# Kernel tuning notes

Hardware: AMD Instinct MI355X
Metric: run time of the kernel (lower is better)

## Reference

```python
import jax, jax.numpy as jnp
import numpy as np

T, B, I, H = 2048, 4096, 3, 5  # seq_len, batch, input_size, hidden_size (from module)


def setup_inputs() -> dict:
    key = jax.random.key(0)
    ks = jax.random.split(key, 10)
    k = 1.0 / np.sqrt(H)  # torch nn.RNN default init bound
    u = lambda kk, shape: jax.random.uniform(kk, shape, jnp.float32, -k, k)
    return {
        "x": jax.random.normal(ks[0], (T, B, I), jnp.float32),
        "hx": jax.random.normal(ks[1], (2, B, H), jnp.float32),
        "w_ih0": u(ks[2], (H, I)),
        "w_hh0": u(ks[3], (H, H)),
        "b_ih0": u(ks[4], (H,)),
        "b_hh0": u(ks[5], (H,)),
        "w_ih1": u(ks[6], (H, H)),
        "w_hh1": u(ks[7], (H, H)),
        "b_ih1": u(ks[8], (H,)),
        "b_hh1": u(ks[9], (H,)),
    }


def reference(x, hx, w_ih0, w_hh0, b_ih0, b_hh0, w_ih1, w_hh1, b_ih1, b_hh1):
    # Precompute layer-0 input projections for all timesteps in one big GEMM.
    pre0 = jnp.einsum("tbi,hi->tbh", x, w_ih0) + b_ih0  # [T, B, H]

    def step(carry, p0_t):
        h0, h1 = carry
        h0 = jnp.tanh(p0_t + h0 @ w_hh0.T + b_hh0)
        h1 = jnp.tanh(h0 @ w_ih1.T + b_ih1 + h1 @ w_hh1.T + b_hh1)
        return (h0, h1), h1

    (h0_f, h1_f), out = jax.lax.scan(step, (hx[0], hx[1]), pre0)
    h_n = jnp.stack([h0_f, h1_f])  # [2, B, H]
    return out, h_n
```

## Files before the change

### kernel.cpp

```cpp
#include <hip/hip_runtime.h>


typedef float v2f  __attribute__((ext_vector_type(2)));
typedef float v2fu __attribute__((ext_vector_type(2), aligned(4)));
typedef float v3fu __attribute__((ext_vector_type(3), aligned(4)));

#define SEQ_T 2048
#define BATCH 4096
#define ISZ 3
#define HSZ 5
#define TBLK 8
#define NSUP (SEQ_T / TBLK)
#define XSTRIDE (BATCH * ISZ)
#define OSTRIDE (BATCH * HSZ)

template<int K>
__device__ __forceinline__ float qbcast(float v) {
    return __int_as_float(__builtin_amdgcn_mov_dpp(
        __float_as_int(v), K * 0x55, 0xF, 0xF, false));
}
__device__ __forceinline__ v2f vsplat(float s) { return (v2f){s, s}; }
__device__ __forceinline__ v2f vfma(float s, v2f w, v2f a) {
    return __builtin_elementwise_fma(vsplat(s), w, a);
}

__global__ __launch_bounds__(128, 1)
void rnn2_pc(const float* __restrict__ x, const float* __restrict__ hx,
             const float* __restrict__ w_ih0, const float* __restrict__ w_hh0,
             const float* __restrict__ b_ih0, const float* __restrict__ b_hh0,
             const float* __restrict__ w_ih1, const float* __restrict__ w_hh1,
             const float* __restrict__ b_ih1, const float* __restrict__ b_hh1,
             float* __restrict__ out)
{
    __shared__ float ring[2][TBLK][16][12];

    const int tid  = threadIdx.x;
    const int wid  = tid >> 6;
    const int lane = tid & 63;
    const int cl   = lane >> 2;
    const int ja   = lane & 3;
    const int jb   = ja + 1;
    const int c    = blockIdx.x * 16 + cl;
    const float S  = 2.8853900817779268f;

    const v2f bias0p = (v2f){ S * (b_ih0[ja] + b_hh0[ja]), S * (b_ih0[jb] + b_hh0[jb]) };
    const v2f bias1p = (v2f){ S * (b_ih1[ja] + b_hh1[ja]), S * (b_ih1[jb] + b_hh1[jb]) };
#define LW(W, k, n)  (v2f){ S * W[ja * (n) + (k)], S * W[jb * (n) + (k)] }
    const v2f wi0p0 = LW(w_ih0, 0, ISZ), wi0p1 = LW(w_ih0, 1, ISZ), wi0p2 = LW(w_ih0, 2, ISZ);
    const v2f wh0p0 = LW(w_hh0, 0, HSZ), wh0p1 = LW(w_hh0, 1, HSZ), wh0p2 = LW(w_hh0, 2, HSZ),
              wh0p3 = LW(w_hh0, 3, HSZ), wh0p4 = LW(w_hh0, 4, HSZ);
    const v2f wi1p0 = LW(w_ih1, 0, HSZ), wi1p1 = LW(w_ih1, 1, HSZ), wi1p2 = LW(w_ih1, 2, HSZ),
              wi1p3 = LW(w_ih1, 3, HSZ), wi1p4 = LW(w_ih1, 4, HSZ);
    const v2f wh1p0 = LW(w_hh1, 0, HSZ), wh1p1 = LW(w_hh1, 1, HSZ), wh1p2 = LW(w_hh1, 2, HSZ),
              wh1p3 = LW(w_hh1, 3, HSZ), wh1p4 = LW(w_hh1, 4, HSZ);
#undef LW

    float h0b0 = hx[(size_t)c * HSZ + 0], h0b1 = hx[(size_t)c * HSZ + 1],
          h0b2 = hx[(size_t)c * HSZ + 2], h0b3 = hx[(size_t)c * HSZ + 3],
          h0b4 = hx[(size_t)c * HSZ + 4];
    const size_t hb1 = (size_t)BATCH * HSZ + (size_t)c * HSZ;
    float h1b0 = hx[hb1 + 0], h1b1 = hx[hb1 + 1], h1b2 = hx[hb1 + 2],
          h1b3 = hx[hb1 + 3], h1b4 = hx[hb1 + 4];

    unsigned xoff = (unsigned)c * ISZ;
    v3fu xA0, xA1, xA2, xA3, xA4, xA5, xA6, xA7;
    v3fu xB0, xB1, xB2, xB3, xB4, xB5, xB6, xB7;
#define LOADX(P)                                                           \
    {                                                                      \
        P##0 = *(const v3fu*)(x + xoff + 0*XSTRIDE);                       \
        P##1 = *(const v3fu*)(x + xoff + 1*XSTRIDE);                       \
        P##2 = *(const v3fu*)(x + xoff + 2*XSTRIDE);                       \
        P##3 = *(const v3fu*)(x + xoff + 3*XSTRIDE);                       \
        P##4 = *(const v3fu*)(x + xoff + 4*XSTRIDE);                       \
        P##5 = *(const v3fu*)(x + xoff + 5*XSTRIDE);                       \
        P##6 = *(const v3fu*)(x + xoff + 6*XSTRIDE);                       \
        P##7 = *(const v3fu*)(x + xoff + 7*XSTRIDE);                       \
        xoff += 8u * XSTRIDE;                                              \
    }

    unsigned ooff = (unsigned)c * HSZ + (unsigned)ja;
    float g0, g1, g2, g3, g4;

#define STEP0(XV, WR, TT)                                                  \
    {                                                                      \
        v2f a = bias0p, cc = (v2f){0.0f, 0.0f};                            \
        a  = vfma(XV.x,  wi0p0, a);                                        \
        cc = vfma(XV.y,  wi0p1, cc);                                       \
        a  = vfma(XV.z,  wi0p2, a);                                        \
        cc = vfma(h0b0, wh0p0, cc);                                        \
        a  = vfma(h0b1, wh0p1, a);                                         \
        cc = vfma(h0b2, wh0p2, cc);                                        \
        a  = vfma(h0b3, wh0p3, a);                                         \
        cc = vfma(h0b4, wh0p4, cc);                                        \
        a = a + cc;                                                        \
        v2f e0;                                                            \
        e0.x = __builtin_amdgcn_exp2f(a.x);                                \
        e0.y = __builtin_amdgcn_exp2f(a.y);                                \
        const v2f p0 = e0 + vsplat(1.0f);                                  \
        v2f r0;                                                            \
        r0.x = __builtin_amdgcn_rcpf(p0.x);                                \
        r0.y = __builtin_amdgcn_rcpf(p0.y);                                \
        const v2f n0 = __builtin_elementwise_fma(vsplat(-2.0f), r0, vsplat(1.0f)); \
        h0b0 = qbcast<0>(n0.x);                                            \
        h0b1 = qbcast<1>(n0.x);                                            \
        h0b2 = qbcast<2>(n0.x);                                            \
        h0b3 = qbcast<3>(n0.x);                                            \
        h0b4 = qbcast<3>(n0.y);                                            \
        *(v2f*)&WR[TT][cl][ja * 2] = n0;                                   \
    }

#define PBLOCK(P, RB)                                                      \
    {                                                                      \
        float (*wr)[16][12] = ring[RB];                                    \
        STEP0(P##0, wr, 0)                                                 \
        STEP0(P##1, wr, 1)                                                 \
        STEP0(P##2, wr, 2)                                                 \
        STEP0(P##3, wr, 3)                                                 \
        STEP0(P##4, wr, 4)                                                 \
        STEP0(P##5, wr, 5)                                                 \
        STEP0(P##6, wr, 6)                                                 \
        STEP0(P##7, wr, 7)                                                 \
    }

#define STEP1(RD, TT, DOPRE)                                               \
    {                                                                      \
        const float u0 = g0, u1 = g1, u2 = g2, u3 = g3, u4 = g4;           \
        if (DOPRE) {                                                       \
            g0 = RD[(TT) + 1][cl][0];                                      \
            g1 = RD[(TT) + 1][cl][2];                                      \
            g2 = RD[(TT) + 1][cl][4];                                      \
            g3 = RD[(TT) + 1][cl][6];                                      \
            g4 = RD[(TT) + 1][cl][7];                                      \
        }                                                                  \
        v2f d = bias1p, ee = (v2f){0.0f, 0.0f};                            \
        d  = vfma(u0,   wi1p0, d);                                         \
        ee = vfma(u1,   wi1p1, ee);                                        \
        d  = vfma(u2,   wi1p2, d);                                         \
        ee = vfma(u3,   wi1p3, ee);                                        \
        d  = vfma(u4,   wi1p4, d);                                         \
        ee = vfma(h1b0, wh1p0, ee);                                        \
        d  = vfma(h1b1, wh1p1, d);                                         \
        ee = vfma(h1b2, wh1p2, ee);                                        \
        d  = vfma(h1b3, wh1p3, d);                                         \
        ee = vfma(h1b4, wh1p4, ee);                                        \
        d = d + ee;                                                        \
        v2f e1;                                                            \
        e1.x = __builtin_amdgcn_exp2f(d.x);                                \
        e1.y = __builtin_amdgcn_exp2f(d.y);                                \
        const v2f p1 = e1 + vsplat(1.0f);                                  \
        v2f r1;                                                            \
        r1.x = __builtin_amdgcn_rcpf(p1.x);                                \
        r1.y = __builtin_amdgcn_rcpf(p1.y);                                \
        const v2f n1 = __builtin_elementwise_fma(vsplat(-2.0f), r1, vsplat(1.0f)); \
        *(v2fu*)(out + ooff) = n1;                                         \
        ooff += OSTRIDE;                                                   \
        h1b0 = qbcast<0>(n1.x);                                            \
        h1b1 = qbcast<1>(n1.x);                                            \
        h1b2 = qbcast<2>(n1.x);                                            \
        h1b3 = qbcast<3>(n1.x);                                            \
        h1b4 = qbcast<3>(n1.y);                                            \
    }

#define CBLOCK(RB)                                                         \
    {                                                                      \
        const float (*rd)[16][12] = ring[RB];                              \
        g0 = rd[0][cl][0];                                                 \
        g1 = rd[0][cl][2];                                                 \
        g2 = rd[0][cl][4];                                                 \
        g3 = rd[0][cl][6];                                                 \
        g4 = rd[0][cl][7];                                                 \
        STEP1(rd, 0, 1)                                                    \
        STEP1(rd, 1, 1)                                                    \
        STEP1(rd, 2, 1)                                                    \
        STEP1(rd, 3, 1)                                                    \
        STEP1(rd, 4, 1)                                                    \
        STEP1(rd, 5, 1)                                                    \
        STEP1(rd, 6, 1)                                                    \
        STEP1(rd, 7, 0)                                                    \
    }

    LOADX(xA)

    __syncthreads();
    if (wid == 0) { LOADX(xB) PBLOCK(xA, 0) }

    for (int sp = 0; sp < 127; ++sp) {
        __syncthreads();
        if (wid == 0) { LOADX(xA) PBLOCK(xB, 1) } else { CBLOCK(0) }
        __syncthreads();
        if (wid == 0) { LOADX(xB) PBLOCK(xA, 0) } else { CBLOCK(1) }
    }

    __syncthreads();
    if (wid == 0) { PBLOCK(xB, 1) } else { CBLOCK(0) }

    __syncthreads();
    if (wid != 0) { CBLOCK(1) }

#undef STEP0
#undef STEP1
#undef PBLOCK
#undef CBLOCK
#undef LOADX

    float* hn = out + (size_t)SEQ_T * BATCH * HSZ;
    if (wid == 0) {
        hn[(size_t)c * HSZ + 0] = h0b0;
        hn[(size_t)c * HSZ + 1] = h0b1;
        hn[(size_t)c * HSZ + 2] = h0b2;
        hn[(size_t)c * HSZ + 3] = h0b3;
        hn[(size_t)c * HSZ + 4] = h0b4;
    } else {
        hn[hb1 + 0] = h1b0;
        hn[hb1 + 1] = h1b1;
        hn[hb1 + 2] = h1b2;
        hn[hb1 + 3] = h1b3;
        hn[hb1 + 4] = h1b4;
    }
}

extern "C" void kernel_launch(void* const* d_in, const int* in_sizes, int n_in,
                              void* d_out, int out_size, void* d_ws, size_t ws_size,
                              hipStream_t stream) {
    rnn2_pc<<<BATCH / 16, 128, 0, stream>>>(
        (const float*)d_in[0], (const float*)d_in[1],
        (const float*)d_in[2], (const float*)d_in[3],
        (const float*)d_in[4], (const float*)d_in[5],
        (const float*)d_in[6], (const float*)d_in[7],
        (const float*)d_in[8], (const float*)d_in[9],
        (float*)d_out);
}
```

Before: 403.7 us.

## Defer layer-1 output stores and double-buffer vectorized LDS prefetch

The layer-1 consumer wave now keeps each block's eight output vectors in registers and writes them to global memory at the start of the next block, so the stores no longer sit inside the serial recurrence chain. The LDS reads of layer-0 hidden states are also reorganized: three 2-wide loads replace five scalar loads, and two register sets alternate so the prefetch runs two steps ahead. This shortens the critical path per timestep at the cost of extra registers and a bunched burst of stores per block.

```diff
diff --git a/kernel.cpp b/kernel.cpp
--- a/kernel.cpp
+++ b/kernel.cpp
@@ -10,7 +10,6 @@
 #define ISZ 3
 #define HSZ 5
 #define TBLK 8
-#define NSUP (SEQ_T / TBLK)
 #define XSTRIDE (BATCH * ISZ)
 #define OSTRIDE (BATCH * HSZ)
 
@@ -25,12 +24,12 @@
 }
 
 __global__ __launch_bounds__(128, 1)
-void rnn2_pc(const float* __restrict__ x, const float* __restrict__ hx,
-             const float* __restrict__ w_ih0, const float* __restrict__ w_hh0,
-             const float* __restrict__ b_ih0, const float* __restrict__ b_hh0,
-             const float* __restrict__ w_ih1, const float* __restrict__ w_hh1,
-             const float* __restrict__ b_ih1, const float* __restrict__ b_hh1,
-             float* __restrict__ out)
+void rnn2_pc2(const float* __restrict__ x, const float* __restrict__ hx,
+              const float* __restrict__ w_ih0, const float* __restrict__ w_hh0,
+              const float* __restrict__ b_ih0, const float* __restrict__ b_hh0,
+              const float* __restrict__ w_ih1, const float* __restrict__ w_hh1,
+              const float* __restrict__ b_ih1, const float* __restrict__ b_hh1,
+              float* __restrict__ out)
 {
     __shared__ float ring[2][TBLK][16][12];
 
@@ -79,7 +78,8 @@
     }
 
     unsigned ooff = (unsigned)c * HSZ + (unsigned)ja;
-    float g0, g1, g2, g3, g4;
+    v2f gA01, gA23, gA34, gB01, gB23, gB34;
+    v2f s0, s1, s2, s3, s4, s5, s6, s7;
 
 #define STEP0(XV, WR, TT)                                                  \
     {                                                                      \
@@ -122,15 +122,14 @@
         STEP0(P##7, wr, 7)                                                 \
     }
 
-#define STEP1(RD, TT, DOPRE)                                               \
-    {                                                                      \
-        const float u0 = g0, u1 = g1, u2 = g2, u3 = g3, u4 = g4;           \
+#define STEP1(UG01, UG23, UG34, RD, PT, DOPRE, SREG)                       \
+    {                                                                      \
+        const float u0 = UG01.x, u1 = UG01.y, u2 = UG23.x,                 \
+                    u3 = UG23.y, u4 = UG34.y;                              \
         if (DOPRE) {                                                       \
-            g0 = RD[(TT) + 1][cl][0];                                      \
-            g1 = RD[(TT) + 1][cl][2];                                      \
-            g2 = RD[(TT) + 1][cl][4];                                      \
-            g3 = RD[(TT) + 1][cl][6];                                      \
-            g4 = RD[(TT) + 1][cl][7];                                      \
+            UG01 = *(const v2f*)&RD[PT][cl][0];                            \
+            UG23 = *(const v2f*)&RD[PT][cl][4];                            \
+            UG34 = *(const v2f*)&RD[PT][cl][6];                            \
         }                                                                  \
         v2f d = bias1p, ee = (v2f){0.0f, 0.0f};                            \
         d  = vfma(u0,   wi1p0, d);                                         \
@@ -152,8 +151,7 @@
         r1.x = __builtin_amdgcn_rcpf(p1.x);                                \
         r1.y = __builtin_amdgcn_rcpf(p1.y);                                \
         const v2f n1 = __builtin_elementwise_fma(vsplat(-2.0f), r1, vsplat(1.0f)); \
-        *(v2fu*)(out + ooff) = n1;                                         \
-        ooff += OSTRIDE;                                                   \
+        SREG = n1;                                                         \
         h1b0 = qbcast<0>(n1.x);                                            \
         h1b1 = qbcast<1>(n1.x);                                            \
         h1b2 = qbcast<2>(n1.x);                                            \
@@ -161,46 +159,65 @@
         h1b4 = qbcast<3>(n1.y);                                            \
     }
 
-#define CBLOCK(RB)                                                         \
+#define FLUSH()                                                            \
+    {                                                                      \
+        *(v2fu*)(out + ooff) = s0; ooff += OSTRIDE;                        \
+        *(v2fu*)(out + ooff) = s1; ooff += OSTRIDE;                        \
+        *(v2fu*)(out + ooff) = s2; ooff += OSTRIDE;                        \
+        *(v2fu*)(out + ooff) = s3; ooff += OSTRIDE;                        \
+        *(v2fu*)(out + ooff) = s4; ooff += OSTRIDE;                        \
+        *(v2fu*)(out + ooff) = s5; ooff += OSTRIDE;                        \
+        *(v2fu*)(out + ooff) = s6; ooff += OSTRIDE;                        \
+        *(v2fu*)(out + ooff) = s7; ooff += OSTRIDE;                        \
+    }
+
+#define CBLOCK(RB, DOFLUSH)                                                \
     {                                                                      \
         const float (*rd)[16][12] = ring[RB];                              \
-        g0 = rd[0][cl][0];                                                 \
-        g1 = rd[0][cl][2];                                                 \
-        g2 = rd[0][cl][4];                                                 \
-        g3 = rd[0][cl][6];                                                 \
-        g4 = rd[0][cl][7];                                                 \
-        STEP1(rd, 0, 1)                                                    \
-        STEP1(rd, 1, 1)                                                    \
-        STEP1(rd, 2, 1)                                                    \
-        STEP1(rd, 3, 1)                                                    \
-        STEP1(rd, 4, 1)                                                    \
-        STEP1(rd, 5, 1)                                                    \
-        STEP1(rd, 6, 1)                                                    \
-        STEP1(rd, 7, 0)                                                    \
+        gA01 = *(const v2f*)&rd[0][cl][0];                                 \
+        gA23 = *(const v2f*)&rd[0][cl][4];                                 \
+        gA34 = *(const v2f*)&rd[0][cl][6];                                 \
+        gB01 = *(const v2f*)&rd[1][cl][0];                                 \
+        gB23 = *(const v2f*)&rd[1][cl][4];                                 \
+        gB34 = *(const v2f*)&rd[1][cl][6];                                 \
+        if (DOFLUSH) FLUSH()                                               \
+        STEP1(gA01, gA23, gA34, rd, 2, 1, s0)                              \
+        STEP1(gB01, gB23, gB34, rd, 3, 1, s1)                              \
+        STEP1(gA01, gA23, gA34, rd, 4, 1, s2)                              \
+        STEP1(gB01, gB23, gB34, rd, 5, 1, s3)                              \
+        STEP1(gA01, gA23, gA34, rd, 6, 1, s4)                              \
+        STEP1(gB01, gB23, gB34, rd, 7, 1, s5)                              \
+        STEP1(gA01, gA23, gA34, rd, 7, 0, s6)                              \
+        STEP1(gB01, gB23, gB34, rd, 7, 0, s7)                              \
     }
 
     LOADX(xA)
-
     __syncthreads();
     if (wid == 0) { LOADX(xB) PBLOCK(xA, 0) }
 
-    for (int sp = 0; sp < 127; ++sp) {
+    __syncthreads();
+    if (wid == 0) { LOADX(xA) PBLOCK(xB, 1) } else { CBLOCK(0, 0) }
+    __syncthreads();
+    if (wid == 0) { LOADX(xB) PBLOCK(xA, 0) } else { CBLOCK(1, 1) }
+
+    for (int sp = 1; sp < 127; ++sp) {
         __syncthreads();
-        if (wid == 0) { LOADX(xA) PBLOCK(xB, 1) } else { CBLOCK(0) }
+        if (wid == 0) { LOADX(xA) PBLOCK(xB, 1) } else { CBLOCK(0, 1) }
         __syncthreads();
-        if (wid == 0) { LOADX(xB) PBLOCK(xA, 0) } else { CBLOCK(1) }
-    }
-
-    __syncthreads();
-    if (wid == 0) { PBLOCK(xB, 1) } else { CBLOCK(0) }
-
-    __syncthreads();
-    if (wid != 0) { CBLOCK(1) }
+        if (wid == 0) { LOADX(xB) PBLOCK(xA, 0) } else { CBLOCK(1, 1) }
+    }
+
+    __syncthreads();
+    if (wid == 0) { PBLOCK(xB, 1) } else { CBLOCK(0, 1) }
+
+    __syncthreads();
+    if (wid != 0) { CBLOCK(1, 1) FLUSH() }
 
 #undef STEP0
 #undef STEP1
 #undef PBLOCK
 #undef CBLOCK
+#undef FLUSH
 #undef LOADX
 
     float* hn = out + (size_t)SEQ_T * BATCH * HSZ;
@@ -222,7 +239,7 @@
 extern "C" void kernel_launch(void* const* d_in, const int* in_sizes, int n_in,
                               void* d_out, int out_size, void* d_ws, size_t ws_size,
                               hipStream_t stream) {
-    rnn2_pc<<<BATCH / 16, 128, 0, stream>>>(
+    rnn2_pc2<<<BATCH / 16, 128, 0, stream>>>(
         (const float*)d_in[0], (const float*)d_in[1],
         (const float*)d_in[2], (const float*)d_in[3],
         (const float*)d_in[4], (const float*)d_in[5],
```

New measurement: 406.2 us. No clear change (+0.6%).

## Pack four producer/consumer wave pairs per block with 64 batch columns

Applied to the files above, without the earlier changes.

Merges four independent producer/consumer pairs into one 512-thread block, each with its own shared-memory ring slice, cutting the grid from 256 to 64 blocks. The intent is to co-schedule more waves per CU to hide latency of the serial recurrence. It risks leaving most CUs idle and adds wider barriers that synchronize eight waves instead of two.

```diff
diff --git a/kernel.cpp b/kernel.cpp
--- a/kernel.cpp
+++ b/kernel.cpp
@@ -10,7 +10,6 @@
 #define ISZ 3
 #define HSZ 5
 #define TBLK 8
-#define NSUP (SEQ_T / TBLK)
 #define XSTRIDE (BATCH * ISZ)
 #define OSTRIDE (BATCH * HSZ)
 
@@ -24,24 +23,28 @@
     return __builtin_elementwise_fma(vsplat(s), w, a);
 }
 
-__global__ __launch_bounds__(128, 1)
-void rnn2_pc(const float* __restrict__ x, const float* __restrict__ hx,
-             const float* __restrict__ w_ih0, const float* __restrict__ w_hh0,
-             const float* __restrict__ b_ih0, const float* __restrict__ b_hh0,
-             const float* __restrict__ w_ih1, const float* __restrict__ w_hh1,
-             const float* __restrict__ b_ih1, const float* __restrict__ b_hh1,
-             float* __restrict__ out)
+__global__ __launch_bounds__(512, 1)
+void rnn2_pc8(const float* __restrict__ x, const float* __restrict__ hx,
+              const float* __restrict__ w_ih0, const float* __restrict__ w_hh0,
+              const float* __restrict__ b_ih0, const float* __restrict__ b_hh0,
+              const float* __restrict__ w_ih1, const float* __restrict__ w_hh1,
+              const float* __restrict__ b_ih1, const float* __restrict__ b_hh1,
+              float* __restrict__ out)
 {
-    __shared__ float ring[2][TBLK][16][12];
+    __shared__ float ring[4][2][TBLK][16][12];
 
     const int tid  = threadIdx.x;
     const int wid  = tid >> 6;
+    const int role = wid >> 2;
+    const int g    = wid & 3;
     const int lane = tid & 63;
     const int cl   = lane >> 2;
     const int ja   = lane & 3;
     const int jb   = ja + 1;
-    const int c    = blockIdx.x * 16 + cl;
+    const int c    = blockIdx.x * 64 + g * 16 + cl;
     const float S  = 2.8853900817779268f;
+
+    float (*rg)[TBLK][16][12] = ring[g];
 
     const v2f bias0p = (v2f){ S * (b_ih0[ja] + b_hh0[ja]), S * (b_ih0[jb] + b_hh0[jb]) };
     const v2f bias1p = (v2f){ S * (b_ih1[ja] + b_hh1[ja]), S * (b_ih1[jb] + b_hh1[jb]) };
@@ -111,7 +114,7 @@
 
 #define PBLOCK(P, RB)                                                      \
     {                                                                      \
-        float (*wr)[16][12] = ring[RB];                                    \
+        float (*wr)[16][12] = rg[RB];                                      \
         STEP0(P##0, wr, 0)                                                 \
         STEP0(P##1, wr, 1)                                                 \
         STEP0(P##2, wr, 2)                                                 \
@@ -163,7 +166,7 @@
 
 #define CBLOCK(RB)                                                         \
     {                                                                      \
-        const float (*rd)[16][12] = ring[RB];                              \
+        const float (*rd)[16][12] = rg[RB];                                \
         g0 = rd[0][cl][0];                                                 \
         g1 = rd[0][cl][2];                                                 \
         g2 = rd[0][cl][4];                                                 \
@@ -179,23 +182,23 @@
         STEP1(rd, 7, 0)                                                    \
     }
 
-    LOADX(xA)
+    if (role == 0) { LOADX(xA) }
 
     __syncthreads();
-    if (wid == 0) { LOADX(xB) PBLOCK(xA, 0) }
+    if (role == 0) { LOADX(xB) PBLOCK(xA, 0) }
 
     for (int sp = 0; sp < 127; ++sp) {
         __syncthreads();
-        if (wid == 0) { LOADX(xA) PBLOCK(xB, 1) } else { CBLOCK(0) }
+        if (role == 0) { LOADX(xA) PBLOCK(xB, 1) } else { CBLOCK(0) }
         __syncthreads();
-        if (wid == 0) { LOADX(xB) PBLOCK(xA, 0) } else { CBLOCK(1) }
+        if (role == 0) { LOADX(xB) PBLOCK(xA, 0) } else { CBLOCK(1) }
     }
 
     __syncthreads();
-    if (wid == 0) { PBLOCK(xB, 1) } else { CBLOCK(0) }
+    if (role == 0) { PBLOCK(xB, 1) } else { CBLOCK(0) }
 
     __syncthreads();
-    if (wid != 0) { CBLOCK(1) }
+    if (role != 0) { CBLOCK(1) }
 
 #undef STEP0
 #undef STEP1
@@ -204,7 +207,7 @@
 #undef LOADX
 
     float* hn = out + (size_t)SEQ_T * BATCH * HSZ;
-    if (wid == 0) {
+    if (role == 0) {
         hn[(size_t)c * HSZ + 0] = h0b0;
         hn[(size_t)c * HSZ + 1] = h0b1;
         hn[(size_t)c * HSZ + 2] = h0b2;
@@ -222,7 +225,7 @@
 extern "C" void kernel_launch(void* const* d_in, const int* in_sizes, int n_in,
                               void* d_out, int out_size, void* d_ws, size_t ws_size,
                               hipStream_t stream) {
-    rnn2_pc<<<BATCH / 16, 128, 0, stream>>>(
+    rnn2_pc8<<<BATCH / 64, 512, 0, stream>>>(
         (const float*)d_in[0], (const float*)d_in[1],
         (const float*)d_in[2], (const float*)d_in[3],
         (const float*)d_in[4], (const float*)d_in[5],
```

Measured after the change: 469.6 us. 1.16x slower.
